# Optimization experiments

Hardware: AMD Instinct MI355X
Metric: run time of the kernel (lower is better)

Reference implementation:

```python
import jax, jax.numpy as jnp
import numpy as np
from jax import lax

B, N, D, H, K = 4096, 25, 256, 8, 3  # batch*frames, nodes, d_model, heads, conv kernel


def _layernorm(x, g, b, eps=1e-5):
    mu = jnp.mean(x, axis=-1, keepdims=True)
    var = jnp.var(x, axis=-1, keepdims=True)
    return (x - mu) * lax.rsqrt(var + eps) * g + b


def _conv1d(x_bdn, w):
    # x_bdn: [B, D, N], w: [D_out, D_in, K], padding=K//2 (same as torch Conv1d)
    return lax.conv_general_dilated(x_bdn, w, window_strides=(1,),
                                    padding=[(K // 2, K // 2)],
                                    dimension_numbers=('NCH', 'OIH', 'NCH'))


def setup_inputs() -> dict:
    key = jax.random.key(0)
    ks = jax.random.split(key, 12)
    x = jax.random.normal(ks[0], (B, N, D), dtype=jnp.float32)
    # symmetric adjacency with self-loops (skeleton graph surrogate)
    a = jax.random.bernoulli(ks[1], 0.3, (N, N))
    adj = a | a.T | jnp.eye(N, dtype=bool)
    cs = 1.0 / np.sqrt(D * K)
    wq = jax.random.normal(ks[2], (D, D, K), dtype=jnp.float32) * cs
    wk = jax.random.normal(ks[3], (D, D, K), dtype=jnp.float32) * cs
    wv = jax.random.normal(ks[4], (D, D, K), dtype=jnp.float32) * cs
    gq = jnp.ones((D,), jnp.float32); bq = jnp.zeros((D,), jnp.float32)
    gk = jnp.ones((D,), jnp.float32); bk = jnp.zeros((D,), jnp.float32)
    gv = jnp.ones((D,), jnp.float32); bv = jnp.zeros((D,), jnp.float32)
    rel_table = jax.random.normal(ks[5], (2 * N - 1, H), dtype=jnp.float32) * 0.02
    local_bias = jnp.zeros((H, N, N), jnp.float32)
    wo = jax.random.normal(ks[6], (D, D), dtype=jnp.float32) * (1.0 / np.sqrt(D))
    bo = jnp.zeros((D,), jnp.float32)
    return dict(x=x, adj=adj, wq=wq, wk=wk, wv=wv, gq=gq, bq=bq, gk=gk, bk=bk,
                gv=gv, bv=bv, rel_table=rel_table, local_bias=local_bias, wo=wo, bo=bo)


def reference(x, adj, wq, wk, wv, gq, bq, gk, bk, gv, bv, rel_table, local_bias, wo, bo):
    b, n, d = x.shape
    h = local_bias.shape[0]
    dk = d // h
    xp = x.transpose(0, 2, 1)  # [B, D, N]
    # conv QKV projection over node axis + per-projection LayerNorm + residual
    q = x + _layernorm(_conv1d(xp, wq).transpose(0, 2, 1), gq, bq)
    k = x + _layernorm(_conv1d(xp, wk).transpose(0, 2, 1), gk, bk)
    v = x + _layernorm(_conv1d(xp, wv).transpose(0, 2, 1), gv, bv)
    qh = q.reshape(b, n, h, dk).transpose(0, 2, 1, 3)  # [B, H, N, dk]
    kh = k.reshape(b, n, h, dk).transpose(0, 2, 1, 3)
    vh = v.reshape(b, n, h, dk).transpose(0, 2, 1, 3)
    scores = jnp.einsum('bhnd,bhmd->bhnm', qh, kh) / np.sqrt(dk)
    # relative positional bias over node indices
    coords = jnp.arange(n)
    idx = coords[:, None] - coords[None, :] + n - 1  # [N, N]
    rel = rel_table[idx].transpose(2, 0, 1)  # [H, N, N]
    scores = scores + rel[None] + local_bias[None]
    # adjacency mask (local attention): non-neighbors -> -inf
    scores = jnp.where(adj[None, None], scores, jnp.finfo(scores.dtype).min)
    attn = jax.nn.softmax(scores, axis=-1)
    out = jnp.einsum('bhnm,bhmd->bhnd', attn, vh)  # [B, H, N, dk]
    out = out.transpose(0, 2, 1, 3).reshape(b, n, d)
    return out @ wo.T + bo
```

## Files before the change

### kernel.cpp

```cpp
#include <hip/hip_runtime.h>

#define BB 4096
#define NN 25
#define DD 256
#define HH 8
#define DKH 32
#define MM (BB*NN)

typedef __bf16 bf16;
typedef bf16 bf16x8 __attribute__((ext_vector_type(8)));
typedef bf16 bf16x4 __attribute__((ext_vector_type(4)));
typedef float f32x4 __attribute__((ext_vector_type(4)));
typedef float f32x16 __attribute__((ext_vector_type(16)));
typedef int   i32x4 __attribute__((ext_vector_type(4)));
typedef _Float16 h16;
typedef h16 h16x2 __attribute__((ext_vector_type(2)));
typedef h16 h16x4 __attribute__((ext_vector_type(4)));
typedef h16 h16x8 __attribute__((ext_vector_type(8)));

__device__ __forceinline__ void async_load16(const void* g, void* l) {
  __builtin_amdgcn_global_load_lds(
      (const __attribute__((address_space(1))) unsigned int*)g,
      (__attribute__((address_space(3))) unsigned int*)l, 16, 0, 0);
}

#define SCHED_FENCE() __builtin_amdgcn_sched_barrier(0)
#define BARRIER() do { SCHED_FENCE(); __builtin_amdgcn_s_barrier(); SCHED_FENCE(); } while (0)

__global__ __launch_bounds__(256) void k_prep(
    const float* __restrict__ x, bf16* __restrict__ xpad,
    const float* __restrict__ wq, const float* __restrict__ wk, const float* __restrict__ wv,
    const float* __restrict__ rel, const float* __restrict__ lb, const float* __restrict__ wo,
    const void* __restrict__ adj_raw,
    bf16* __restrict__ Wt, h16* __restrict__ woF, float* __restrict__ mbF2) {
  if (blockIdx.x < 13824) {
    int idx = (blockIdx.x * 256 + threadIdx.x) * 8;
    const int total = BB * 27 * 256;
    if (idx >= total) return;
    int b = idx / (27 * 256);
    int rem = idx - b * 27 * 256;
    int j = rem >> 8;
    int d = rem & 255;
    bf16x8 o;
    if (j >= 1 && j <= 25) {
      const float* src = x + ((b * 25 + (j - 1)) * 256 + d);
      #pragma unroll
      for (int t = 0; t < 8; ++t) o[t] = (bf16)src[t];
    } else {
      #pragma unroll
      for (int t = 0; t < 8; ++t) o[t] = (bf16)0.0f;
    }
    *(bf16x8*)(xpad + idx) = o;
    return;
  }
  const unsigned char* abytes = (const unsigned char*)adj_raw;
  bool anyb = false;
  {
    const int ln = threadIdx.x & 63;
    #pragma unroll
    for (int t = 0; t < 10; ++t) {
      int s = ln + t * 64;
      if (s < 625 && (s & 3) && abytes[s]) anyb = true;
    }
  }
  const bool u8 = __any(anyb);

  const int NWT = 768 * 768;
  const int NMB = HH * 64 * 16;
  const int NWF = 8 * 16 * 64 * 8;
  const int total = NWT + NMB + NWF;
  for (int i = (blockIdx.x - 13824) * 256 + threadIdx.x; i < total; i += 512 * 256) {
    if (i < NWT) {
      int j = i / 768, kk = i - j * 768;
      int proj = j >> 8, jo = j & 255;
      int tap = kk >> 8, di = kk & 255;
      const float* w = (proj == 0) ? wq : ((proj == 1) ? wk : wv);
      Wt[i] = (bf16)w[(jo * 256 + di) * 3 + tap];
    } else if (i < NWT + NMB) {
      int t = i - NWT;
      int h = t >> 10;
      int L = (t >> 4) & 63;
      int r = t & 15;
      int iq = L & 31;
      int m = (r & 3) + 8 * (r >> 2) + 4 * (L >> 5);
      float v;
      if (m >= 25) {
        v = -1e30f;
      } else if (iq >= 25) {
        v = 0.0f;
      } else {
        int amask = u8 ? (abytes[iq * 25 + m] ? 1 : 0)
                       : (((const int*)adj_raw)[iq * 25 + m] ? 1 : 0);
        v = amask ? (rel[(iq - m + 24) * HH + h] + lb[h * 625 + iq * 25 + m]) : -1e30f;
      }
      mbF2[t] = v;
    } else {
      int e = i - NWT - NMB;
      int c = e & 7, ln = (e >> 3) & 63, nt = (e >> 9) & 15, ks = e >> 13;
      int col = nt * 16 + (ln & 15);
      int k = ks * 32 + (ln >> 4) * 8 + c;
      woF[e] = (h16)wo[col * 256 + k];
    }
  }
}

__global__ __launch_bounds__(512, 2) void k_qkv_gemm8(const bf16* __restrict__ xpad,
                                                      const bf16* __restrict__ Wt,
                                                      bf16* __restrict__ conv) {
  __shared__ bf16 Ab[2][256 * 64];
  __shared__ bf16 Bb[2][256 * 64];

  const int L = blockIdx.x;
  const int sw = (L & 7) * 150 + (L >> 3);
  const int n0 = (sw % 3) * 256;
  const int m0 = (sw / 3) * 256;

  const int tid = threadIdx.x;
  const int lane = tid & 63, wave = tid >> 6;
  const int t16 = lane & 15, quad = lane >> 4;
  const int wr = wave >> 2, wc = wave & 3;

  const int srow = tid >> 3;
  const int sc = ((tid & 7) << 4) ^ ((srow & 7) << 4);
  int aOff[4], bOff[4];
  #pragma unroll
  for (int q = 0; q < 4; ++q) {
    int row = q * 64 + srow;
    int gm = m0 + row;
    int b = gm / 25;
    int n = gm - b * 25;
    aOff[q] = (b * 27 + n) * 512 + sc;
    bOff[q] = (n0 + row) * 1536 + sc;
  }

  const int axr = (t16 & 7) << 3;
  int aoffs[2], boffs[2];
  #pragma unroll
  for (int kk = 0; kk < 2; ++kk) {
    aoffs[kk] = (wr * 128 + t16) * 64 + ((kk * 32 + quad * 8) ^ axr);
    boffs[kk] = (wc * 64 + t16) * 64 + ((kk * 32 + quad * 8) ^ axr);
  }

  f32x4 acc[8][4];
  #pragma unroll
  for (int i = 0; i < 8; ++i)
    #pragma unroll
    for (int j = 0; j < 4; ++j) acc[i][j] = (f32x4){0.f, 0.f, 0.f, 0.f};

  #define ST_B(bufi, tt) do {                                              \
    char* lb_ = (char*)&Bb[bufi][0] + wave * 1024;                         \
    _Pragma("unroll")                                                      \
    for (int q_ = 0; q_ < 4; ++q_)                                         \
      async_load16((const char*)Wt + bOff[q_] + (tt) * 128, lb_ + q_ * 8192); \
  } while (0)
  #define ST_A(bufi, tt) do {                                              \
    char* la_ = (char*)&Ab[bufi][0] + wave * 1024;                         \
    const int ka_ = ((tt) >> 2) * 512 + ((tt) & 3) * 128;                  \
    _Pragma("unroll")                                                      \
    for (int q_ = 0; q_ < 4; ++q_)                                         \
      async_load16((const char*)xpad + aOff[q_] + ka_, la_ + q_ * 8192);   \
  } while (0)

  ST_B(0, 0); ST_A(0, 0);
  ST_B(1, 1); ST_A(1, 1);
  asm volatile("s_waitcnt vmcnt(8)" ::: "memory");
  SCHED_FENCE();
  BARRIER();

  bf16x8 aLo[8], aHi[8], bLo[4], bHi[4];
  {
    const bf16* Ac = &Ab[0][0];
    const bf16* Bc = &Bb[0][0];
    #pragma unroll
    for (int i = 0; i < 4; ++i)
      #pragma unroll
      for (int kk = 0; kk < 2; ++kk)
        aLo[i * 2 + kk] = *(const bf16x8*)(Ac + aoffs[kk] + i * 1024);
    #pragma unroll
    for (int j = 0; j < 2; ++j)
      #pragma unroll
      for (int kk = 0; kk < 2; ++kk)
        bLo[j * 2 + kk] = *(const bf16x8*)(Bc + boffs[kk] + j * 1024);
  }
  SCHED_FENCE();

  for (int u = 0; u < 12; ++u) {
    const int buf = u & 1;
    const bf16* Ac = &Ab[buf][0];
    const bf16* Bc = &Bb[buf][0];
    const bf16* Ac2 = &Ab[buf ^ 1][0];
    const bf16* Bc2 = &Bb[buf ^ 1][0];
    const int st = u + 2;

    #pragma unroll
    for (int j = 0; j < 2; ++j)
      #pragma unroll
      for (int kk = 0; kk < 2; ++kk)
        bHi[j * 2 + kk] = *(const bf16x8*)(Bc + boffs[kk] + (2 + j) * 1024);
    SCHED_FENCE();
    __builtin_amdgcn_s_setprio(1);
    #pragma unroll
    for (int i = 0; i < 4; ++i)
      #pragma unroll
      for (int j = 0; j < 2; ++j)
        #pragma unroll
        for (int kk = 0; kk < 2; ++kk)
          acc[i][j] = __builtin_amdgcn_mfma_f32_16x16x32_bf16(
              aLo[i * 2 + kk], bLo[j * 2 + kk], acc[i][j], 0, 0, 0);
    __builtin_amdgcn_s_setprio(0);
    SCHED_FENCE();

    #pragma unroll
    for (int i = 0; i < 4; ++i)
      #pragma unroll
      for (int kk = 0; kk < 2; ++kk)
        aHi[i * 2 + kk] = *(const bf16x8*)(Ac + aoffs[kk] + (4 + i) * 1024);
    SCHED_FENCE();
    __builtin_amdgcn_s_setprio(1);
    #pragma unroll
    for (int i = 0; i < 4; ++i)
      #pragma unroll
      for (int j = 0; j < 2; ++j)
        #pragma unroll
        for (int kk = 0; kk < 2; ++kk)
          acc[i][2 + j] = __builtin_amdgcn_mfma_f32_16x16x32_bf16(
              aLo[i * 2 + kk], bHi[j * 2 + kk], acc[i][2 + j], 0, 0, 0);
    __builtin_amdgcn_s_setprio(0);
    SCHED_FENCE();

    BARRIER();
    if (st < 12) ST_B(buf, st);
    SCHED_FENCE();
    __builtin_amdgcn_s_setprio(1);
    #pragma unroll
    for (int i = 0; i < 4; ++i)
      #pragma unroll
      for (int j = 0; j < 2; ++j)
        #pragma unroll
        for (int kk = 0; kk < 2; ++kk)
          acc[4 + i][j] = __builtin_amdgcn_mfma_f32_16x16x32_bf16(
              aHi[i * 2 + kk], bLo[j * 2 + kk], acc[4 + i][j], 0, 0, 0);
    __builtin_amdgcn_s_setprio(0);
    SCHED_FENCE();

    if (u < 11) {
      if (u < 10) {
        asm volatile("s_waitcnt vmcnt(4)" ::: "memory");
      } else {
        asm volatile("s_waitcnt vmcnt(0)" ::: "memory");
      }
      SCHED_FENCE();
      BARRIER();
      if (st < 12) ST_A(buf, st);
      #pragma unroll
      for (int i = 0; i < 4; ++i)
        #pragma unroll
        for (int kk = 0; kk < 2; ++kk)
          aLo[i * 2 + kk] = *(const bf16x8*)(Ac2 + aoffs[kk] + i * 1024);
      #pragma unroll
      for (int j = 0; j < 2; ++j)
        #pragma unroll
        for (int kk = 0; kk < 2; ++kk)
          bLo[j * 2 + kk] = *(const bf16x8*)(Bc2 + boffs[kk] + j * 1024);
      SCHED_FENCE();
    }
    __builtin_amdgcn_s_setprio(1);
    #pragma unroll
    for (int i = 0; i < 4; ++i)
      #pragma unroll
      for (int j = 0; j < 2; ++j)
        #pragma unroll
        for (int kk = 0; kk < 2; ++kk)
          acc[4 + i][2 + j] = __builtin_amdgcn_mfma_f32_16x16x32_bf16(
              aHi[i * 2 + kk], bHi[j * 2 + kk], acc[4 + i][2 + j], 0, 0, 0);
    __builtin_amdgcn_s_setprio(0);
    SCHED_FENCE();
  }
  #undef ST_A
  #undef ST_B

  #pragma unroll
  for (int i = 0; i < 8; ++i)
    #pragma unroll
    for (int j = 0; j < 4; ++j) {
      const int col = n0 + wc * 64 + j * 16 + t16;
      #pragma unroll
      for (int r = 0; r < 4; ++r) {
        const int rowm = m0 + wr * 128 + i * 16 + quad * 4 + r;
        conv[(size_t)rowm * 768 + col] = (bf16)acc[i][j][r];
      }
    }
}

__global__ __launch_bounds__(256, 4) void k_attn_oproj(
    const bf16* __restrict__ conv, const float* __restrict__ x,
    const float* __restrict__ gq, const float* __restrict__ bq,
    const float* __restrict__ gk, const float* __restrict__ bk,
    const float* __restrict__ gv, const float* __restrict__ bv,
    const float* __restrict__ mbF2, const h16* __restrict__ woF,
    const float* __restrict__ bo, float* __restrict__ out) {
  __shared__ bf16 Cs[19456];
  const int b = blockIdx.x;
  const int tid = threadIdx.x;
  const int wave = tid >> 6, lane = tid & 63;

  const char* slab = (const char*)(conv + (size_t)b * 19200);
  for (int c = wave; c < 38; c += 4)
    async_load16(slab + c * 1024 + lane * 16, (char*)Cs + c * 1024);

  h16x4 xpre[19];
  #pragma unroll
  for (int k = 0; k < 19; ++k) {
    const int rowi = wave + 4 * k;
    if (rowi < 75) {
      const int n = rowi / 3;
      f32x4 xv = *(const f32x4*)(x + ((size_t)(b * 25 + n)) * 256 + lane * 4);
      h16x4 t;
      t[0] = (h16)xv[0]; t[1] = (h16)xv[1]; t[2] = (h16)xv[2]; t[3] = (h16)xv[3];
      xpre[k] = t;
    } else {
      xpre[k] = (h16x4){(h16)0.f, (h16)0.f, (h16)0.f, (h16)0.f};
    }
  }

  asm volatile("s_waitcnt vmcnt(0)" ::: "memory");
  __syncthreads();

  #pragma unroll
  for (int k = 0; k < 19; ++k) {
    const int rowi = wave + 4 * k;
    if (rowi < 75) {
      const int n = rowi / 3;
      const int p = rowi - n * 3;
      const int rbyte = n * 1536 + p * 512 + lane * 8;
      bf16x4 cv = *(const bf16x4*)((const char*)Cs + rbyte);
      float v0 = (float)cv[0], v1 = (float)cv[1], v2 = (float)cv[2], v3 = (float)cv[3];
      float s = v0 + v1 + v2 + v3;
      float ss = v0 * v0 + v1 * v1 + v2 * v2 + v3 * v3;
      #pragma unroll
      for (int o = 32; o; o >>= 1) {
        s += __shfl_xor(s, o);
        ss += __shfl_xor(ss, o);
      }
      float mu = s * (1.0f / 256.0f);
      float var = ss * (1.0f / 256.0f) - mu * mu;
      float rs = rsqrtf(var + 1e-5f);
      const float* gsel = (p == 0) ? gq : ((p == 1) ? gk : gv);
      const float* bsel = (p == 0) ? bq : ((p == 1) ? bk : bv);
      const int dbase = lane * 4;
      f32x4 gg = *(const f32x4*)(gsel + dbase);
      f32x4 b2 = *(const f32x4*)(bsel + dbase);
      h16x4 xh = xpre[k];
      h16x4 o;
      o[0] = (h16)((v0 - mu) * rs * gg[0] + b2[0]) + xh[0];
      o[1] = (h16)((v1 - mu) * rs * gg[1] + b2[1]) + xh[1];
      o[2] = (h16)((v2 - mu) * rs * gg[2] + b2[2]) + xh[2];
      o[3] = (h16)((v3 - mu) * rs * gg[3] + b2[3]) + xh[3];
      const int wbyte = n * 1536 + ((p * 512 + lane * 8) ^ ((n & 3) << 4));
      *(h16x4*)((char*)Cs + wbyte) = o;
    }
  }
  __syncthreads();

  {
    const int hi = lane >> 5;
    const int dl = lane & 31;
    const int rowc = dl > 24 ? 24 : dl;
    const char* base = (const char*)Cs;
    const float scale = 0.17677669529663687f;

    #pragma unroll 1
    for (int hh = 0; hh < 2; ++hh) {
      const int h = wave * 2 + hh;

      h16x8 aK[2], bQ[2];
      #pragma unroll
      for (int ks = 0; ks < 2; ++ks) {
        const int kb = h * 64 + ks * 32 + hi * 16;
        aK[ks] = *(const h16x8*)(base + rowc * 1536 + ((512 + kb) ^ ((rowc & 3) << 4)));
        bQ[ks] = *(const h16x8*)(base + rowc * 1536 + ((kb) ^ ((rowc & 3) << 4)));
      }
      f32x16 sacc = (f32x16)(0.0f);
      sacc = __builtin_amdgcn_mfma_f32_32x32x16_f16(aK[0], bQ[0], sacc, 0, 0, 0);
      sacc = __builtin_amdgcn_mfma_f32_32x32x16_f16(aK[1], bQ[1], sacc, 0, 0, 0);

      const float* bp = mbF2 + ((h * 64 + lane) << 4);
      f32x4 b4[4];
      #pragma unroll
      for (int c = 0; c < 4; ++c) b4[c] = *(const f32x4*)(bp + 4 * c);
      float p[16];
      #pragma unroll
      for (int r = 0; r < 16; ++r) p[r] = sacc[r] * scale + b4[r >> 2][r & 3];

      float mx = p[0];
      #pragma unroll
      for (int r = 1; r < 16; ++r) mx = fmaxf(mx, p[r]);
      mx = fmaxf(mx, __shfl_xor(mx, 32));
      float sum = 0.f;
      #pragma unroll
      for (int r = 0; r < 16; ++r) { p[r] = __expf(p[r] - mx); sum += p[r]; }
      sum += __shfl_xor(sum, 32);
      const float inv = 1.0f / sum;
      #pragma unroll
      for (int r = 0; r < 16; ++r) p[r] *= inv;

      int c8[8], d8[8];
      #pragma unroll
      for (int k2 = 0; k2 < 8; ++k2) {
        h16x2 t;
        t[0] = (h16)p[2 * k2];
        t[1] = (h16)p[2 * k2 + 1];
        c8[k2] = __builtin_bit_cast(int, t);
      }
      #pragma unroll
      for (int k2 = 0; k2 < 8; ++k2) d8[k2] = __shfl_xor(c8[k2], 32);
      i32x4 f0 = hi ? (i32x4){d8[2], d8[3], c8[2], c8[3]}
                    : (i32x4){c8[0], c8[1], d8[0], d8[1]};
      i32x4 f1 = hi ? (i32x4){d8[6], d8[7], c8[6], c8[7]}
                    : (i32x4){c8[4], c8[5], d8[4], d8[5]};
      h16x8 fragP0 = __builtin_bit_cast(h16x8, f0);
      h16x8 fragP1 = __builtin_bit_cast(h16x8, f1);

      h16x8 vb0, vb1;
      #pragma unroll
      for (int c = 0; c < 8; ++c) {
        const int m0v = hi * 8 + c;
        int m1v = 16 + hi * 8 + c;
        if (m1v > 24) m1v = 24;
        const int cb = 1024 + h * 64 + 2 * dl;
        vb0[c] = *(const h16*)(base + m0v * 1536 + (cb ^ ((m0v & 3) << 4)));
        vb1[c] = *(const h16*)(base + m1v * 1536 + (cb ^ ((m1v & 3) << 4)));
      }

      f32x16 oacc = (f32x16)(0.0f);
      oacc = __builtin_amdgcn_mfma_f32_32x32x16_f16(fragP0, vb0, oacc, 0, 0, 0);
      oacc = __builtin_amdgcn_mfma_f32_32x32x16_f16(fragP1, vb1, oacc, 0, 0, 0);

      #pragma unroll
      for (int r = 0; r < 16; ++r) {
        const int io = (r & 3) + 8 * (r >> 2) + 4 * hi;
        if (io < 25) {
          const int wb = io * 1536 + ((h * 64 + 2 * dl) ^ ((io & 3) << 4));
          *(h16*)((char*)Cs + wb) = (h16)oacc[r];
        }
      }
    }
  }
  __syncthreads();

  {
    const int t16 = lane & 15, quad = lane >> 4;
    f32x4 oacc[2][4];
    #pragma unroll
    for (int mt = 0; mt < 2; ++mt)
      #pragma unroll
      for (int jj = 0; jj < 4; ++jj) oacc[mt][jj] = (f32x4){0.f, 0.f, 0.f, 0.f};
    const int arow0 = t16;
    const int arow1 = (16 + t16 > 24) ? 24 : 16 + t16;
    #pragma unroll
    for (int ks = 0; ks < 8; ++ks) {
      h16x8 aF0, aF1;
      {
        const int kb = ks * 64 + quad * 16;
        aF0 = *(const h16x8*)((const char*)Cs + arow0 * 1536 + (kb ^ ((arow0 & 3) << 4)));
        aF1 = *(const h16x8*)((const char*)Cs + arow1 * 1536 + (kb ^ ((arow1 & 3) << 4)));
      }
      #pragma unroll
      for (int jj = 0; jj < 4; ++jj) {
        const h16x8 bF = *(const h16x8*)(woF + ((ks * 16 + wave * 4 + jj) << 9) + lane * 8);
        oacc[0][jj] = __builtin_amdgcn_mfma_f32_16x16x32_f16(aF0, bF, oacc[0][jj], 0, 0, 0);
        oacc[1][jj] = __builtin_amdgcn_mfma_f32_16x16x32_f16(aF1, bF, oacc[1][jj], 0, 0, 0);
      }
    }
    #pragma unroll
    for (int jj = 0; jj < 4; ++jj) {
      const int col = (wave * 4 + jj) * 16 + t16;
      const float bb = bo[col];
      #pragma unroll
      for (int mt = 0; mt < 2; ++mt)
        #pragma unroll
        for (int r = 0; r < 4; ++r) {
          const int row = mt * 16 + quad * 4 + r;
          if (row < 25)
            out[((size_t)b * 25 + row) * 256 + col] = oacc[mt][jj][r] + bb;
        }
    }
  }
}

extern "C" void kernel_launch(void* const* d_in, const int* in_sizes, int n_in,
                              void* d_out, int out_size, void* d_ws, size_t ws_size,
                              hipStream_t stream) {
  (void)in_sizes; (void)n_in; (void)out_size; (void)ws_size;
  const float* x  = (const float*)d_in[0];
  const void*  adj = d_in[1];
  const float* wq = (const float*)d_in[2];
  const float* wk = (const float*)d_in[3];
  const float* wv = (const float*)d_in[4];
  const float* gq = (const float*)d_in[5];
  const float* bq = (const float*)d_in[6];
  const float* gk = (const float*)d_in[7];
  const float* bk = (const float*)d_in[8];
  const float* gv = (const float*)d_in[9];
  const float* bv = (const float*)d_in[10];
  const float* rel = (const float*)d_in[11];
  const float* lb = (const float*)d_in[12];
  const float* wo = (const float*)d_in[13];
  const float* bo = (const float*)d_in[14];
  float* out = (float*)d_out;

  char* ws = (char*)d_ws;
  size_t off = 0;
  auto alloc = [&](size_t bytes) -> void* {
    void* p = ws + off;
    off += (bytes + 255) & ~(size_t)255;
    return p;
  };
  bf16* xpad = (bf16*)alloc((size_t)BB * 27 * 256 * 2);
  bf16* conv = (bf16*)alloc((size_t)MM * 768 * 2);
  bf16* Wt   = (bf16*)alloc((size_t)768 * 768 * 2);
  h16*  woF  = (h16*)alloc((size_t)65536 * 2);
  float* mbF2 = (float*)alloc((size_t)HH * 64 * 16 * 4);

  hipLaunchKernelGGL(k_prep, dim3(14336), dim3(256), 0, stream,
                     x, xpad, wq, wk, wv, rel, lb, wo, adj, Wt, woF, mbF2);
  hipLaunchKernelGGL(k_qkv_gemm8, dim3(1200), dim3(512), 0, stream, xpad, Wt, conv);
  hipLaunchKernelGGL(k_attn_oproj, dim3(4096), dim3(256), 0, stream,
                     conv, x, gq, bq, gk, bk, gv, bv, mbF2, woF, bo, out);
}
```

Baseline: 459.6 us.

## Fuse LayerNorm and residual into QKV GEMM epilogue, widen prep conversion

The per-projection LayerNorm and residual add move from the attention kernel into the QKV GEMM epilogue. Row sums and sums of squares are reduced across lanes and waves through shared memory, and the final fp16 values are written already swizzled. The attention kernel then only async-loads the slab, which drops its x reads and normalisation pass. Separately, the prep kernel converts 16 elements per thread with vectorised float4 loads. The epilogue now does scalar 2-byte scattered stores and scalar x reads, which may be less coalesced than before.

```diff
diff --git a/kernel.cpp b/kernel.cpp
--- a/kernel.cpp
+++ b/kernel.cpp
@@ -33,24 +33,29 @@
     const float* __restrict__ rel, const float* __restrict__ lb, const float* __restrict__ wo,
     const void* __restrict__ adj_raw,
     bf16* __restrict__ Wt, h16* __restrict__ woF, float* __restrict__ mbF2) {
-  if (blockIdx.x < 13824) {
-    int idx = (blockIdx.x * 256 + threadIdx.x) * 8;
-    const int total = BB * 27 * 256;
-    if (idx >= total) return;
-    int b = idx / (27 * 256);
-    int rem = idx - b * 27 * 256;
+  if (blockIdx.x < 6912) {
+    int idx = (blockIdx.x * 256 + threadIdx.x) * 16;
+    int b = idx / 6912;
+    int rem = idx - b * 6912;
     int j = rem >> 8;
     int d = rem & 255;
-    bf16x8 o;
+    bf16x8 o0, o1;
     if (j >= 1 && j <= 25) {
       const float* src = x + ((b * 25 + (j - 1)) * 256 + d);
-      #pragma unroll
-      for (int t = 0; t < 8; ++t) o[t] = (bf16)src[t];
+      f32x4 v0 = *(const f32x4*)(src);
+      f32x4 v1 = *(const f32x4*)(src + 4);
+      f32x4 v2 = *(const f32x4*)(src + 8);
+      f32x4 v3 = *(const f32x4*)(src + 12);
+      #pragma unroll
+      for (int t = 0; t < 4; ++t) { o0[t] = (bf16)v0[t]; o0[4 + t] = (bf16)v1[t]; }
+      #pragma unroll
+      for (int t = 0; t < 4; ++t) { o1[t] = (bf16)v2[t]; o1[4 + t] = (bf16)v3[t]; }
     } else {
       #pragma unroll
-      for (int t = 0; t < 8; ++t) o[t] = (bf16)0.0f;
-    }
-    *(bf16x8*)(xpad + idx) = o;
+      for (int t = 0; t < 8; ++t) { o0[t] = (bf16)0.0f; o1[t] = (bf16)0.0f; }
+    }
+    *(bf16x8*)(xpad + idx) = o0;
+    *(bf16x8*)(xpad + idx + 8) = o1;
     return;
   }
   const unsigned char* abytes = (const unsigned char*)adj_raw;
@@ -69,7 +74,7 @@
   const int NMB = HH * 64 * 16;
   const int NWF = 8 * 16 * 64 * 8;
   const int total = NWT + NMB + NWF;
-  for (int i = (blockIdx.x - 13824) * 256 + threadIdx.x; i < total; i += 512 * 256) {
+  for (int i = (blockIdx.x - 6912) * 256 + threadIdx.x; i < total; i += 512 * 256) {
     if (i < NWT) {
       int j = i / 768, kk = i - j * 768;
       int proj = j >> 8, jo = j & 255;
@@ -104,9 +109,13 @@
   }
 }
 
-__global__ __launch_bounds__(512, 2) void k_qkv_gemm8(const bf16* __restrict__ xpad,
-                                                      const bf16* __restrict__ Wt,
-                                                      bf16* __restrict__ conv) {
+__global__ __launch_bounds__(512, 2) void k_qkv_gemm8(
+    const bf16* __restrict__ xpad, const bf16* __restrict__ Wt,
+    const float* __restrict__ x,
+    const float* __restrict__ gq, const float* __restrict__ bq,
+    const float* __restrict__ gk, const float* __restrict__ bk,
+    const float* __restrict__ gv, const float* __restrict__ bv,
+    h16* __restrict__ conv) {
   __shared__ bf16 Ab[2][256 * 64];
   __shared__ bf16 Bb[2][256 * 64];
 
@@ -279,27 +288,67 @@
   #undef ST_A
   #undef ST_B
 
+  BARRIER();
+  float* Ps = (float*)&Ab[0][0];
+  float* Qs = Ps + 1024;
   #pragma unroll
   for (int i = 0; i < 8; ++i)
     #pragma unroll
-    for (int j = 0; j < 4; ++j) {
-      const int col = n0 + wc * 64 + j * 16 + t16;
-      #pragma unroll
-      for (int r = 0; r < 4; ++r) {
-        const int rowm = m0 + wr * 128 + i * 16 + quad * 4 + r;
-        conv[(size_t)rowm * 768 + col] = (bf16)acc[i][j][r];
+    for (int r = 0; r < 4; ++r) {
+      float s  = acc[i][0][r] + acc[i][1][r] + acc[i][2][r] + acc[i][3][r];
+      float ss = acc[i][0][r] * acc[i][0][r] + acc[i][1][r] * acc[i][1][r]
+               + acc[i][2][r] * acc[i][2][r] + acc[i][3][r] * acc[i][3][r];
+      #pragma unroll
+      for (int o = 1; o < 16; o <<= 1) { s += __shfl_xor(s, o); ss += __shfl_xor(ss, o); }
+      if (t16 == 0) {
+        const int row = wr * 128 + i * 16 + quad * 4 + r;
+        Ps[row * 4 + wc] = s;
+        Qs[row * 4 + wc] = ss;
+      }
+    }
+  BARRIER();
+  const int proj = n0 >> 8;
+  const float* gsel = (proj == 0) ? gq : ((proj == 1) ? gk : gv);
+  const float* bsel = (proj == 0) ? bq : ((proj == 1) ? bk : bv);
+  float gv4[4], bv4[4];
+  #pragma unroll
+  for (int j = 0; j < 4; ++j) {
+    const int col = wc * 64 + j * 16 + t16;
+    gv4[j] = gsel[col];
+    bv4[j] = bsel[col];
+  }
+  #pragma unroll
+  for (int i = 0; i < 8; ++i)
+    #pragma unroll
+    for (int r = 0; r < 4; ++r) {
+      const int row = wr * 128 + i * 16 + quad * 4 + r;
+      const int gm = m0 + row;
+      const int bb_ = gm / 25;
+      const int n = gm - bb_ * 25;
+      f32x4 sv = *(const f32x4*)(Ps + row * 4);
+      f32x4 qv2 = *(const f32x4*)(Qs + row * 4);
+      const float S  = sv[0] + sv[1] + sv[2] + sv[3];
+      const float SS = qv2[0] + qv2[1] + qv2[2] + qv2[3];
+      const float mu = S * (1.0f / 256.0f);
+      const float var = SS * (1.0f / 256.0f) - mu * mu;
+      const float rs = rsqrtf(var + 1e-5f);
+      const int swz = (n & 3) << 4;
+      char* rowbase = (char*)conv + (size_t)gm * 1536 + proj * 512;
+      #pragma unroll
+      for (int j = 0; j < 4; ++j) {
+        const int col = wc * 64 + j * 16 + t16;
+        const float xv = x[(size_t)gm * 256 + col];
+        const float val = (acc[i][j][r] - mu) * rs * gv4[j] + bv4[j] + xv;
+        *(h16*)(rowbase + ((col * 2) ^ swz)) = (h16)val;
       }
     }
 }
 
 __global__ __launch_bounds__(256, 4) void k_attn_oproj(
-    const bf16* __restrict__ conv, const float* __restrict__ x,
-    const float* __restrict__ gq, const float* __restrict__ bq,
-    const float* __restrict__ gk, const float* __restrict__ bk,
-    const float* __restrict__ gv, const float* __restrict__ bv,
+    const h16* __restrict__ conv,
     const float* __restrict__ mbF2, const h16* __restrict__ woF,
     const float* __restrict__ bo, float* __restrict__ out) {
-  __shared__ bf16 Cs[19456];
+  __shared__ h16 Cs[19456];
   const int b = blockIdx.x;
   const int tid = threadIdx.x;
   const int wave = tid >> 6, lane = tid & 63;
@@ -307,59 +356,7 @@
   const char* slab = (const char*)(conv + (size_t)b * 19200);
   for (int c = wave; c < 38; c += 4)
     async_load16(slab + c * 1024 + lane * 16, (char*)Cs + c * 1024);
-
-  h16x4 xpre[19];
-  #pragma unroll
-  for (int k = 0; k < 19; ++k) {
-    const int rowi = wave + 4 * k;
-    if (rowi < 75) {
-      const int n = rowi / 3;
-      f32x4 xv = *(const f32x4*)(x + ((size_t)(b * 25 + n)) * 256 + lane * 4);
-      h16x4 t;
-      t[0] = (h16)xv[0]; t[1] = (h16)xv[1]; t[2] = (h16)xv[2]; t[3] = (h16)xv[3];
-      xpre[k] = t;
-    } else {
-      xpre[k] = (h16x4){(h16)0.f, (h16)0.f, (h16)0.f, (h16)0.f};
-    }
-  }
-
   asm volatile("s_waitcnt vmcnt(0)" ::: "memory");
-  __syncthreads();
-
-  #pragma unroll
-  for (int k = 0; k < 19; ++k) {
-    const int rowi = wave + 4 * k;
-    if (rowi < 75) {
-      const int n = rowi / 3;
-      const int p = rowi - n * 3;
-      const int rbyte = n * 1536 + p * 512 + lane * 8;
-      bf16x4 cv = *(const bf16x4*)((const char*)Cs + rbyte);
-      float v0 = (float)cv[0], v1 = (float)cv[1], v2 = (float)cv[2], v3 = (float)cv[3];
-      float s = v0 + v1 + v2 + v3;
-      float ss = v0 * v0 + v1 * v1 + v2 * v2 + v3 * v3;
-      #pragma unroll
-      for (int o = 32; o; o >>= 1) {
-        s += __shfl_xor(s, o);
-        ss += __shfl_xor(ss, o);
-      }
-      float mu = s * (1.0f / 256.0f);
-      float var = ss * (1.0f / 256.0f) - mu * mu;
-      float rs = rsqrtf(var + 1e-5f);
-      const float* gsel = (p == 0) ? gq : ((p == 1) ? gk : gv);
-      const float* bsel = (p == 0) ? bq : ((p == 1) ? bk : bv);
-      const int dbase = lane * 4;
-      f32x4 gg = *(const f32x4*)(gsel + dbase);
-      f32x4 b2 = *(const f32x4*)(bsel + dbase);
-      h16x4 xh = xpre[k];
-      h16x4 o;
-      o[0] = (h16)((v0 - mu) * rs * gg[0] + b2[0]) + xh[0];
-      o[1] = (h16)((v1 - mu) * rs * gg[1] + b2[1]) + xh[1];
-      o[2] = (h16)((v2 - mu) * rs * gg[2] + b2[2]) + xh[2];
-      o[3] = (h16)((v3 - mu) * rs * gg[3] + b2[3]) + xh[3];
-      const int wbyte = n * 1536 + ((p * 512 + lane * 8) ^ ((n & 3) << 4));
-      *(h16x4*)((char*)Cs + wbyte) = o;
-    }
-  }
   __syncthreads();
 
   {
@@ -517,14 +514,15 @@
     return p;
   };
   bf16* xpad = (bf16*)alloc((size_t)BB * 27 * 256 * 2);
-  bf16* conv = (bf16*)alloc((size_t)MM * 768 * 2);
+  h16*  conv = (h16*)alloc((size_t)MM * 768 * 2);
   bf16* Wt   = (bf16*)alloc((size_t)768 * 768 * 2);
   h16*  woF  = (h16*)alloc((size_t)65536 * 2);
   float* mbF2 = (float*)alloc((size_t)HH * 64 * 16 * 4);
 
-  hipLaunchKernelGGL(k_prep, dim3(14336), dim3(256), 0, stream,
+  hipLaunchKernelGGL(k_prep, dim3(7424), dim3(256), 0, stream,
                      x, xpad, wq, wk, wv, rel, lb, wo, adj, Wt, woF, mbF2);
-  hipLaunchKernelGGL(k_qkv_gemm8, dim3(1200), dim3(512), 0, stream, xpad, Wt, conv);
+  hipLaunchKernelGGL(k_qkv_gemm8, dim3(1200), dim3(512), 0, stream,
+                     xpad, Wt, x, gq, bq, gk, bk, gv, bv, conv);
   hipLaunchKernelGGL(k_attn_oproj, dim3(4096), dim3(256), 0, stream,
-                     conv, x, gq, bq, gk, bk, gv, bv, mbF2, woF, bo, out);
+                     conv, mbF2, woF, bo, out);
 }
```

After: 478.3 us. 4.1% more time.
